# Performance work log

Hardware: AMD Instinct MI355X
Metric: run time of the kernel (lower is better)

The kernel has to match this reference:

```python
import jax, jax.numpy as jnp
import numpy as np

K = 4        # kernel_size
PAD = 2      # padding
GROUPS = 1   # groups


def _unfold(x, H, W):
    # x: [B, C, Hp, Wp] padded map; stride-1 KxK windows, sliced to first HxW
    # positions (matches torch unfold(2,K,1).unfold(3,K,1)[:, :, :H, :W]).
    # Returns [B, C, H, W, K*K].
    return jnp.stack([x[:, :, i:i + H, j:j + W]
                      for i in range(K) for j in range(K)], axis=-1)


def setup_inputs() -> dict:
    key = jax.random.key(0)
    ks = jax.random.split(key, 7)
    B, Cin, H, W, Cout = 8, 3, 128, 128, 64
    c = Cout // GROUPS
    return {
        "x": jax.random.normal(ks[0], (B, Cin, H, W), jnp.float32),
        "q_w": jax.random.normal(ks[1], (Cout, Cin), jnp.float32) * 0.2,
        "k_w": jax.random.normal(ks[2], (Cout, Cin), jnp.float32) * 0.2,
        "v_w": jax.random.normal(ks[3], (Cout, Cin), jnp.float32) * 0.2,
        "emb_a": jax.random.normal(ks[4], (c, W), jnp.float32),
        "emb_b": jax.random.normal(ks[5], (c, H), jnp.float32),
        "emb_mix": jax.random.normal(ks[6], (c, H, W), jnp.float32),
    }


def reference(x, q_w, k_w, v_w, emb_a, emb_b, emb_mix):
    B, Cin, H, W = x.shape
    O = q_w.shape[0]
    G = GROUPS
    c = O // G
    KK = K * K

    # 1x1 convs (no bias) as channel contractions
    q = jnp.einsum('oc,bchw->bohw', q_w, x)                      # [B,O,H,W]
    xp = jnp.pad(x, ((0, 0), (0, 0), (PAD, PAD), (PAD, PAD)))
    k = jnp.einsum('oc,bchw->bohw', k_w, xp)                     # [B,O,Hp,Wp]
    v = jnp.einsum('oc,bchw->bohw', v_w, xp)

    # im2col-style local windows -> [B,G,c,H,W,KK]
    k = _unfold(k, H, W).reshape(B, G, c, H, W, KK)
    v = _unfold(v, H, W).reshape(B, G, c, H, W, KK)

    # positional embedding logits (elementwise scale of v per (c,h,w))
    logit_a = v * emb_a[None, None, :, None, :, None]            # 'bnchwk,cw'
    logit_b = v * emb_b[None, None, :, :, None, None]            # 'bnchwk,ch'
    logit_mix = v * emb_mix[None, None, :, :, :, None]           # 'bnchwk,chw'
    embedding = jax.nn.softmax((logit_a + logit_b) * logit_mix, axis=-1)

    qr = q.reshape(B, G, c, H, W, 1)
    att = jax.nn.softmax(qr * k * embedding, axis=-1)            # double softmax
    out = jnp.sum(att * v, axis=-1).reshape(B, O, H, W)
    return out
```

## Files before the change

### kernel.cpp

```cpp
#include <hip/hip_runtime.h>

typedef float f2 __attribute__((ext_vector_type(2)));
typedef float f4 __attribute__((ext_vector_type(4)));

static __device__ __forceinline__ f2 vmax2(f2 a, f2 b) {
  f2 r;
  r.x = fmaxf(a.x, b.x); r.y = fmaxf(a.y, b.y);
  return r;
}
static __device__ __forceinline__ f2 vexp2(f2 a) {
  f2 r;
  r.x = __builtin_amdgcn_exp2f(a.x);
  r.y = __builtin_amdgcn_exp2f(a.y);
  return r;
}

__global__ __launch_bounds__(256, 4) void stem_kernel(
    const float* __restrict__ x,
    const float* __restrict__ qwp,
    const float* __restrict__ kwp,
    const float* __restrict__ vwp,
    const float* __restrict__ ea,
    const float* __restrict__ eb,
    const float* __restrict__ em,
    float* __restrict__ out)
{
  __shared__ float xt[3][132][4];

  const int blk = blockIdx.x;
  const int cc = blk & 1;
  const int h  = (blk >> 1) & 127;
  const int b  = blk >> 8;
  const int t  = threadIdx.x;

  for (int idx = t; idx < 3 * 4 * 132; idx += 256) {
    int wp  = idx % 132;
    int rem = idx / 132;
    int rr  = rem & 3;
    int cin = rem >> 2;
    int sr = h - 2 + rr;
    int sc = wp - 2;
    float val = 0.0f;
    if ((unsigned)sr < 128u && (unsigned)sc < 128u)
      val = x[((b * 3 + cin) * 128 + sr) * 128 + sc];
    xt[cin][wp][rr] = val;
  }
  __syncthreads();

  const int w  = t & 127;
  const int cg = t >> 7;
  const float LOG2E = 1.4426950408889634f;

  const int base_c = cc * 32 + cg * 16;
#pragma unroll 1
  for (int i = 0; i < 16; ++i) {
    const int c = __builtin_amdgcn_readfirstlane(base_c + i);

    const float kwa = kwp[c * 3 + 0], kwb = kwp[c * 3 + 1], kwc = kwp[c * 3 + 2];
    const float vwa = vwp[c * 3 + 0], vwb = vwp[c * 3 + 1], vwc = vwp[c * 3 + 2];
    const float qwa = qwp[c * 3 + 0], qwb = qwp[c * 3 + 1], qwc = qwp[c * 3 + 2];

    f2 kk[8], vv[8];
    float q = 0.0f;
#pragma unroll
    for (int j = 0; j < 4; ++j) {
      f4 x0 = *(const f4*)(&xt[0][w + j][0]);
      f4 x1 = *(const f4*)(&xt[1][w + j][0]);
      f4 x2 = *(const f4*)(&xt[2][w + j][0]);
      f2 lo0 = f2{x0.x, x0.y}, hi0 = f2{x0.z, x0.w};
      f2 lo1 = f2{x1.x, x1.y}, hi1 = f2{x1.z, x1.w};
      f2 lo2 = f2{x2.x, x2.y}, hi2 = f2{x2.z, x2.w};
      kk[2 * j]     = kwa * lo0 + kwb * lo1 + kwc * lo2;
      kk[2 * j + 1] = kwa * hi0 + kwb * hi1 + kwc * hi2;
      vv[2 * j]     = vwa * lo0 + vwb * lo1 + vwc * lo2;
      vv[2 * j + 1] = vwa * hi0 + vwb * hi1 + vwc * hi2;
      if (j == 2)
        q = qwa * hi0.x + qwb * hi1.x + qwc * hi2.x;
    }

    const float sp =
        (ea[c * 128 + w] + eb[c * 128 + h]) * em[(c * 128 + h) * 128 + w] * LOG2E;

    f2 tl[8];
#pragma unroll
    for (int u = 0; u < 8; ++u) tl[u] = (sp * vv[u]) * vv[u];

    f2 mm = vmax2(vmax2(vmax2(tl[0], tl[1]), vmax2(tl[2], tl[3])),
                  vmax2(vmax2(tl[4], tl[5]), vmax2(tl[6], tl[7])));
    const float tmax = fmaxf(mm.x, mm.y);

#pragma unroll
    for (int u = 0; u < 8; ++u) tl[u] = vexp2(tl[u] - tmax);

    f2 se = ((tl[0] + tl[1]) + (tl[2] + tl[3])) + ((tl[4] + tl[5]) + (tl[6] + tl[7]));
    const float sum_e = se.x + se.y;
    const float qs = q * LOG2E * __builtin_amdgcn_rcpf(sum_e);

    f2 ps = f2{0.0f, 0.0f}, pv = f2{0.0f, 0.0f};
#pragma unroll
    for (int u = 0; u < 8; ++u) {
      f2 p = vexp2((qs * kk[u]) * tl[u]);
      ps = ps + p;
      pv = pv + p * vv[u];
    }

    const float denom = ps.x + ps.y;
    const float numer = pv.x + pv.y;

    out[((b * 64 + c) * 128 + h) * 128 + w] =
        numer * __builtin_amdgcn_rcpf(denom);
  }
}

extern "C" void kernel_launch(void* const* d_in, const int* in_sizes, int n_in,
                              void* d_out, int out_size, void* d_ws, size_t ws_size,
                              hipStream_t stream) {
  const float* x  = (const float*)d_in[0];
  const float* qw = (const float*)d_in[1];
  const float* kw = (const float*)d_in[2];
  const float* vw = (const float*)d_in[3];
  const float* ea = (const float*)d_in[4];
  const float* eb = (const float*)d_in[5];
  const float* em = (const float*)d_in[6];
  float* out = (float*)d_out;

  stem_kernel<<<dim3(8 * 128 * 2), dim3(256), 0, stream>>>(x, qw, kw, vw, ea, eb, em, out);
}
```

Before: 58.80 us.

## Precompute k/v projections into shared memory and split channels across more blocks

Each block now handles 4 channels for one row instead of 32, so the grid grows from 2048 to 16384 blocks. The block first computes the k and v 1x1-conv projections for its padded row window into shared memory, which removes the 4x redundant recomputation of each projection across overlapping windows. The attention loop then reads k and v from LDS. The cost is a much larger grid where every block reloads the 3x4x132 input tile and goes through two extra barriers for only two channels per thread, so fixed per-block overhead rises sharply.

Result: slower. 71.84 us (+22.2%).

```diff
diff --git a/kernel.cpp b/kernel.cpp
--- a/kernel.cpp
+++ b/kernel.cpp
@@ -3,17 +3,14 @@
 typedef float f2 __attribute__((ext_vector_type(2)));
 typedef float f4 __attribute__((ext_vector_type(4)));
 
-static __device__ __forceinline__ f2 vmax2(f2 a, f2 b) {
-  f2 r;
-  r.x = fmaxf(a.x, b.x); r.y = fmaxf(a.y, b.y);
-  return r;
-}
 static __device__ __forceinline__ f2 vexp2(f2 a) {
   f2 r;
   r.x = __builtin_amdgcn_exp2f(a.x);
   r.y = __builtin_amdgcn_exp2f(a.y);
   return r;
 }
+
+#define LOG2E 1.4426950408889634f
 
 __global__ __launch_bounds__(256, 4) void stem_kernel(
     const float* __restrict__ x,
@@ -25,90 +22,98 @@
     const float* __restrict__ em,
     float* __restrict__ out)
 {
-  __shared__ float xt[3][132][4];
+  __shared__ __align__(16) float xs[3][132][4];
+  __shared__ __align__(16) float kv[2][4][132][4];
 
   const int blk = blockIdx.x;
-  const int cc = blk & 1;
-  const int h  = (blk >> 1) & 127;
-  const int b  = blk >> 8;
-  const int t  = threadIdx.x;
+  const int cc  = (blk & 15) * 4;
+  const int h   = (blk >> 4) & 127;
+  const int b   = blk >> 11;
+  const int t   = threadIdx.x;
 
-  for (int idx = t; idx < 3 * 4 * 132; idx += 256) {
+  for (int idx = t; idx < 1584; idx += 256) {
     int wp  = idx % 132;
     int rem = idx / 132;
-    int rr  = rem & 3;
+    int r   = rem & 3;
     int cin = rem >> 2;
-    int sr = h - 2 + rr;
-    int sc = wp - 2;
+    int sr = h - 2 + r, sc = wp - 2;
     float val = 0.0f;
     if ((unsigned)sr < 128u && (unsigned)sc < 128u)
       val = x[((b * 3 + cin) * 128 + sr) * 128 + sc];
-    xt[cin][wp][rr] = val;
+    xs[cin][wp][r] = val;
+  }
+  __syncthreads();
+
+  for (int idx = t; idx < 528; idx += 256) {
+    int wp = idx % 132;
+    int cl = idx / 132;
+    int c  = cc + cl;
+    f4 x0 = *(const f4*)&xs[0][wp][0];
+    f4 x1 = *(const f4*)&xs[1][wp][0];
+    f4 x2 = *(const f4*)&xs[2][wp][0];
+    float ka = kwp[c * 3 + 0], kb = kwp[c * 3 + 1], kc = kwp[c * 3 + 2];
+    float va = vwp[c * 3 + 0], vb = vwp[c * 3 + 1], vc = vwp[c * 3 + 2];
+    f4 km = ka * x0 + kb * x1 + kc * x2;
+    f4 vm = va * x0 + vb * x1 + vc * x2;
+    *(f4*)&kv[0][cl][wp][0] = km;
+    *(f4*)&kv[1][cl][wp][0] = vm;
   }
   __syncthreads();
 
   const int w  = t & 127;
   const int cg = t >> 7;
-  const float LOG2E = 1.4426950408889634f;
 
-  const int base_c = cc * 32 + cg * 16;
+  const float xq0 = xs[0][w + 2][2];
+  const float xq1 = xs[1][w + 2][2];
+  const float xq2 = xs[2][w + 2][2];
+
 #pragma unroll 1
-  for (int i = 0; i < 16; ++i) {
-    const int c = __builtin_amdgcn_readfirstlane(base_c + i);
+  for (int i = 0; i < 2; ++i) {
+    const int cl = cg * 2 + i;
+    const int c  = __builtin_amdgcn_readfirstlane(cc + cl);
 
-    const float kwa = kwp[c * 3 + 0], kwb = kwp[c * 3 + 1], kwc = kwp[c * 3 + 2];
-    const float vwa = vwp[c * 3 + 0], vwb = vwp[c * 3 + 1], vwc = vwp[c * 3 + 2];
-    const float qwa = qwp[c * 3 + 0], qwb = qwp[c * 3 + 1], qwc = qwp[c * 3 + 2];
-
-    f2 kk[8], vv[8];
-    float q = 0.0f;
+    f2 vv[8];
 #pragma unroll
     for (int j = 0; j < 4; ++j) {
-      f4 x0 = *(const f4*)(&xt[0][w + j][0]);
-      f4 x1 = *(const f4*)(&xt[1][w + j][0]);
-      f4 x2 = *(const f4*)(&xt[2][w + j][0]);
-      f2 lo0 = f2{x0.x, x0.y}, hi0 = f2{x0.z, x0.w};
-      f2 lo1 = f2{x1.x, x1.y}, hi1 = f2{x1.z, x1.w};
-      f2 lo2 = f2{x2.x, x2.y}, hi2 = f2{x2.z, x2.w};
-      kk[2 * j]     = kwa * lo0 + kwb * lo1 + kwc * lo2;
-      kk[2 * j + 1] = kwa * hi0 + kwb * hi1 + kwc * hi2;
-      vv[2 * j]     = vwa * lo0 + vwb * lo1 + vwc * lo2;
-      vv[2 * j + 1] = vwa * hi0 + vwb * hi1 + vwc * hi2;
-      if (j == 2)
-        q = qwa * hi0.x + qwb * hi1.x + qwc * hi2.x;
+      f4 v4 = *(const f4*)&kv[1][cl][w + j][0];
+      vv[2 * j]     = f2{v4.x, v4.y};
+      vv[2 * j + 1] = f2{v4.z, v4.w};
     }
 
+    const float q = qwp[c * 3 + 0] * xq0 + qwp[c * 3 + 1] * xq1 +
+                    qwp[c * 3 + 2] * xq2;
     const float sp =
         (ea[c * 128 + w] + eb[c * 128 + h]) * em[(c * 128 + h) * 128 + w] * LOG2E;
 
-    f2 tl[8];
+    f2 e[8];
 #pragma unroll
-    for (int u = 0; u < 8; ++u) tl[u] = (sp * vv[u]) * vv[u];
+    for (int u = 0; u < 8; ++u) e[u] = (sp * vv[u]) * vv[u];
 
-    f2 mm = vmax2(vmax2(vmax2(tl[0], tl[1]), vmax2(tl[2], tl[3])),
-                  vmax2(vmax2(tl[4], tl[5]), vmax2(tl[6], tl[7])));
-    const float tmax = fmaxf(mm.x, mm.y);
+    float tmax = fmaxf(fmaxf(fmaxf(e[0].x, e[0].y), fmaxf(e[1].x, e[1].y)),
+                       fmaxf(fmaxf(e[2].x, e[2].y), fmaxf(e[3].x, e[3].y)));
+    tmax = fmaxf(tmax, fmaxf(fmaxf(e[4].x, e[4].y), fmaxf(e[5].x, e[5].y)));
+    tmax = fmaxf(tmax, fmaxf(fmaxf(e[6].x, e[6].y), fmaxf(e[7].x, e[7].y)));
 
 #pragma unroll
-    for (int u = 0; u < 8; ++u) tl[u] = vexp2(tl[u] - tmax);
+    for (int u = 0; u < 8; ++u) e[u] = vexp2(e[u] - tmax);
 
-    f2 se = ((tl[0] + tl[1]) + (tl[2] + tl[3])) + ((tl[4] + tl[5]) + (tl[6] + tl[7]));
+    f2 se = ((e[0] + e[1]) + (e[2] + e[3])) + ((e[4] + e[5]) + (e[6] + e[7]));
     const float sum_e = se.x + se.y;
     const float qs = q * LOG2E * __builtin_amdgcn_rcpf(sum_e);
 
     f2 ps = f2{0.0f, 0.0f}, pv = f2{0.0f, 0.0f};
 #pragma unroll
-    for (int u = 0; u < 8; ++u) {
-      f2 p = vexp2((qs * kk[u]) * tl[u]);
-      ps = ps + p;
-      pv = pv + p * vv[u];
+    for (int j = 0; j < 4; ++j) {
+      f4 k4 = *(const f4*)&kv[0][cl][w + j][0];
+      f2 p0 = vexp2((qs * f2{k4.x, k4.y}) * e[2 * j]);
+      f2 p1 = vexp2((qs * f2{k4.z, k4.w}) * e[2 * j + 1]);
+      ps = ps + p0 + p1;
+      pv = pv + p0 * vv[2 * j];
+      pv = pv + p1 * vv[2 * j + 1];
     }
 
-    const float denom = ps.x + ps.y;
-    const float numer = pv.x + pv.y;
-
     out[((b * 64 + c) * 128 + h) * 128 + w] =
-        numer * __builtin_amdgcn_rcpf(denom);
+        (pv.x + pv.y) * __builtin_amdgcn_rcpf(ps.x + ps.y);
   }
 }
 
@@ -124,5 +129,5 @@
   const float* em = (const float*)d_in[6];
   float* out = (float*)d_out;
 
-  stem_kernel<<<dim3(8 * 128 * 2), dim3(256), 0, stream>>>(x, qw, kw, vw, ea, eb, em, out);
+  stem_kernel<<<dim3(8 * 128 * 16), dim3(256), 0, stream>>>(x, qw, kw, vw, ea, eb, em, out);
 }
```
